# Optimization experiments

Hardware: AMD Instinct MI355X
Metric: run time of the kernel (lower is better)

The kernel has to match this reference:

```python
import jax, jax.numpy as jnp
import numpy as np

D_MODEL = 2048
NHEADS = 16
HEAD_DIM = D_MODEL // NHEADS


def setup_inputs() -> dict:
    key = jax.random.key(0)
    kx, kq, kk, kv, ko = jax.random.split(key, 5)
    B, S = 2, 2048
    scale = 1.0 / np.sqrt(D_MODEL)
    return {
        "x": jax.random.normal(kx, (B, S, D_MODEL), dtype=jnp.float32),
        "Wq": jax.random.normal(kq, (D_MODEL, D_MODEL), dtype=jnp.float32) * scale,
        "Wk": jax.random.normal(kk, (D_MODEL, D_MODEL), dtype=jnp.float32) * scale,
        "Wv": jax.random.normal(kv, (D_MODEL, D_MODEL), dtype=jnp.float32) * scale,
        "Wo": jax.random.normal(ko, (D_MODEL, D_MODEL), dtype=jnp.float32) * scale,
    }


def reference(x, Wq, Wk, Wv, Wo):
    B, S, _ = x.shape
    # nn.Linear(bias=False): y = x @ W.T
    q = (x @ Wq.T).reshape(B, S, NHEADS, HEAD_DIM)
    k = (x @ Wk.T).reshape(B, S, NHEADS, HEAD_DIM)
    v = (x @ Wv.T).reshape(B, S, NHEADS, HEAD_DIM)
    sm_scale = 1.0 / np.sqrt(HEAD_DIM)
    # scores: [B, H, S, S]
    scores = jnp.einsum("bqhd,bkhd->bhqk", q, k) * sm_scale
    causal_mask = jnp.tril(jnp.ones((S, S), dtype=bool))  # [S, S]
    scores = jnp.where(causal_mask, scores, jnp.finfo(scores.dtype).min)
    probs = jax.nn.softmax(scores, axis=-1)
    attn = jnp.einsum("bhqk,bkhd->bqhd", probs, v)  # [B, S, H, D]
    out = attn.reshape(B, S, D_MODEL) @ Wo.T
    return out
```

## Files before the change

kernel.cpp:

```cpp
#include <hip/hip_runtime.h>
#include <hip/hip_bf16.h>
#include <type_traits>

#define DEV __device__ __forceinline__

typedef __bf16 bf16x8 __attribute__((ext_vector_type(8)));
typedef float f32x4 __attribute__((ext_vector_type(4)));
typedef float f32x16 __attribute__((ext_vector_type(16)));
typedef unsigned short u16;
typedef unsigned int u32;

DEV u16 f32_to_bf16(float f) {
  union { float f; u32 u; } x; x.f = f;
  u32 r = (x.u + 0x7FFFu + ((x.u >> 16) & 1u)) >> 16;
  return (u16)r;
}

DEV u32 pack2(float a, float b) {
  union { __hip_bfloat162 h; u32 u; } c;
  c.h = __float22bfloat162_rn(float2{a, b});
  return c.u;
}

DEV void ld_lds16(const void* g, void* l) {
  __builtin_amdgcn_global_load_lds(
      (const __attribute__((address_space(1))) u32*)g,
      (__attribute__((address_space(3))) u32*)l, 16, 0, 0);
}

#define MFMA16(a, b, c) __builtin_amdgcn_mfma_f32_16x16x32_bf16(a, b, c, 0, 0, 0)
#define MFMA32(a, b, c) __builtin_amdgcn_mfma_f32_32x32x16_bf16(a, b, c, 0, 0, 0)

__global__ __launch_bounds__(256) void cast_kernel(const float* __restrict__ in,
                                                   u16* __restrict__ out, int n) {
  int i = (blockIdx.x * 256 + threadIdx.x) * 4;
  if (i >= n) return;
  float4 v = *reinterpret_cast<const float4*>(in + i);
  ushort4 o;
  o.x = f32_to_bf16(v.x); o.y = f32_to_bf16(v.y);
  o.z = f32_to_bf16(v.z); o.w = f32_to_bf16(v.w);
  *reinterpret_cast<ushort4*>(out + i) = o;
}

template <typename OutT>
__global__ __launch_bounds__(256) void gemm_nt(const u16* __restrict__ A,
                                               const u16* __restrict__ B,
                                               OutT* __restrict__ C,
                                               int M, int N, int K, float osc) {
  __shared__ __align__(16) u16 sA[128 * 64];
  __shared__ __align__(16) u16 sB[128 * 64];
  const int tid = threadIdx.x;
  const int lane = tid & 63, wid = tid >> 6;
  const int lo = lane & 15, hi = lane >> 4;
  const int wm = wid >> 1, wn = wid & 1;
  const int m0 = blockIdx.y * 128, n0 = blockIdx.x * 128;

  f32x4 acc[4][4] = {};

  for (int k0 = 0; k0 < K; k0 += 64) {
    __syncthreads();
#pragma unroll
    for (int i = 0; i < 4; ++i) {
      int e16 = i * 256 + tid;
      int r = e16 >> 3;
      int bcol = ((e16 & 7) * 16) ^ ((r & 7) << 4);
      int col = bcol >> 1;
      ld_lds16(A + (size_t)(m0 + r) * K + k0 + col, sA + e16 * 8);
      ld_lds16(B + (size_t)(n0 + r) * K + k0 + col, sB + e16 * 8);
    }
    __syncthreads();
#pragma unroll
    for (int kc = 0; kc < 2; ++kc) {
      bf16x8 a[4], b[4];
#pragma unroll
      for (int i = 0; i < 4; ++i) {
        int row = wm * 64 + i * 16 + lo;
        int boff = ((kc * 32 + hi * 8) * 2) ^ ((row & 7) << 4);
        a[i] = *(const bf16x8*)((const char*)sA + row * 128 + boff);
      }
#pragma unroll
      for (int i = 0; i < 4; ++i) {
        int row = wn * 64 + i * 16 + lo;
        int boff = ((kc * 32 + hi * 8) * 2) ^ ((row & 7) << 4);
        b[i] = *(const bf16x8*)((const char*)sB + row * 128 + boff);
      }
#pragma unroll
      for (int mi = 0; mi < 4; ++mi)
#pragma unroll
        for (int ni = 0; ni < 4; ++ni)
          acc[mi][ni] = MFMA16(a[mi], b[ni], acc[mi][ni]);
    }
  }
#pragma unroll
  for (int mi = 0; mi < 4; ++mi)
#pragma unroll
    for (int r = 0; r < 4; ++r) {
      size_t row = m0 + wm * 64 + mi * 16 + hi * 4 + r;
#pragma unroll
      for (int ni = 0; ni < 4; ++ni) {
        int col = n0 + wn * 64 + ni * 16 + lo;
        float v = acc[mi][ni][r] * osc;
        if constexpr (std::is_same<OutT, float>::value)
          C[row * N + col] = v;
        else
          C[row * N + col] = f32_to_bf16(v);
      }
    }
}

constexpr float RTHR2 = 11.5416f;

__global__ __launch_bounds__(512, 2) void attn_fwd(const u16* __restrict__ Q,
                                                   const u16* __restrict__ K,
                                                   const u16* __restrict__ VT,
                                                   u16* __restrict__ O) {
  __shared__ __align__(16) u16 sK[2][64 * 128];
  __shared__ __align__(16) u16 sV[2][128 * 64];

  const int p = blockIdx.x, h = blockIdx.y, b = blockIdx.z;
  const int tid = threadIdx.x;
  const int lane = tid & 63, wid = tid >> 6;
  const int l31 = lane & 31, hi5 = lane >> 5;
  const int g = wid >> 2;
  const int qt = g ? p : (15 - p);
  const int qw = qt * 128 + (wid & 3) * 32;
  const int qg = qw + l31;
  const int nt = 2 * (15 - p) + 2;

  const size_t baseQK = ((size_t)b * 2048) * 2048 + (size_t)h * 128;
  const size_t baseV  = ((size_t)h * 128) * 4096 + (size_t)b * 2048;

  bf16x8 qf[8];
#pragma unroll
  for (int kc = 0; kc < 8; ++kc)
    qf[kc] = *(const bf16x8*)(Q + baseQK + (size_t)qg * 2048 + kc * 16 + hi5 * 8);

  f32x16 o[4] = {};
  float m = -INFINITY, ls = 0.f;

  auto stage = [&](int buf, int t) {
    const int kv = t * 64;
#pragma unroll
    for (int i = 0; i < 2; ++i) {
      int e = i * 512 + tid;
      int r = e >> 4;
      int bc = ((e & 15) * 16) ^ ((r & 7) << 4);
      ld_lds16(K + baseQK + (size_t)(kv + r) * 2048 + (bc >> 1), &sK[buf][e * 8]);
    }
#pragma unroll
    for (int i = 0; i < 2; ++i) {
      int e = i * 512 + tid;
      int r = e >> 3;
      int bc = ((e & 7) * 16) ^ ((r & 7) << 4);
      ld_lds16(VT + baseV + (size_t)r * 4096 + kv + (bc >> 1), &sV[buf][e * 8]);
    }
  };

  stage(0, 0);

  for (int t = 0; t < nt; ++t) {
    __syncthreads();
    if (t + 1 < nt) stage((t + 1) & 1, t + 1);
    const int kv0 = t * 64;
    if (kv0 > qw + 31) continue;
    const u16* bK = sK[t & 1];
    const u16* bV = sV[t & 1];

    f32x16 s[2] = {};
    __builtin_amdgcn_s_setprio(1);
#pragma unroll
    for (int kb = 0; kb < 2; ++kb) {
      int row = kb * 32 + l31;
      int rsw = (row & 7) << 4;
#pragma unroll
      for (int kc = 0; kc < 8; ++kc) {
        int bo = (kc * 32 + hi5 * 16) ^ rsw;
        bf16x8 kf = *(const bf16x8*)((const char*)bK + row * 256 + bo);
        s[kb] = MFMA32(kf, qf[kc], s[kb]);
      }
    }
    __builtin_amdgcn_s_setprio(0);

    if (kv0 + 63 > qw) {
#pragma unroll
      for (int kb = 0; kb < 2; ++kb)
#pragma unroll
        for (int j = 0; j < 16; ++j) {
          int keyg = kv0 + kb * 32 + (j & 3) + 8 * (j >> 2) + 4 * hi5;
          s[kb][j] = (keyg > qg) ? -3e38f : s[kb][j];
        }
    }

    float pmax = -3e38f;
#pragma unroll
    for (int kb = 0; kb < 2; ++kb)
#pragma unroll
      for (int j = 0; j < 16; ++j) pmax = fmaxf(pmax, s[kb][j]);
    pmax = fmaxf(pmax, __shfl_xor(pmax, 32));

    if (!__all(pmax - m <= RTHR2)) {
      float mn = fmaxf(m, pmax);
      float fr = exp2f(m - mn);
      ls *= fr;
#pragma unroll
      for (int d = 0; d < 4; ++d) o[d] *= fr;
      m = mn;
    }

    float rs = 0.f;
#pragma unroll
    for (int kb = 0; kb < 2; ++kb)
#pragma unroll
      for (int j = 0; j < 16; ++j) {
        float pv = exp2f(s[kb][j] - m);
        s[kb][j] = pv;
        rs += pv;
      }
    rs += __shfl_xor(rs, 32);
    ls += rs;

    union PF { u32 w[4]; bf16x8 v; };
    PF pf[4];
#pragma unroll
    for (int kb = 0; kb < 2; ++kb)
#pragma unroll
      for (int gp = 0; gp < 2; ++gp) {
        u32 keep[2], send[2];
#pragma unroll
        for (int w = 0; w < 2; ++w) {
          int ja = 8 * gp + 2 * w;
          int jb = 8 * gp + 4 + 2 * w;
          u32 aa = pack2(s[kb][ja], s[kb][ja + 1]);
          u32 bb = pack2(s[kb][jb], s[kb][jb + 1]);
          keep[w] = hi5 ? bb : aa;
          send[w] = hi5 ? aa : bb;
        }
        u32 recv0 = (u32)__shfl_xor((int)send[0], 32);
        u32 recv1 = (u32)__shfl_xor((int)send[1], 32);
        PF& f = pf[2 * kb + gp];
        f.w[0] = hi5 ? recv0 : keep[0];
        f.w[1] = hi5 ? recv1 : keep[1];
        f.w[2] = hi5 ? keep[0] : recv0;
        f.w[3] = hi5 ? keep[1] : recv1;
      }

    __builtin_amdgcn_s_setprio(1);
#pragma unroll
    for (int d = 0; d < 4; ++d) {
      int row = d * 32 + l31;
      int rsw = (row & 7) << 4;
#pragma unroll
      for (int ks = 0; ks < 4; ++ks) {
        int bo = (ks * 32 + hi5 * 16) ^ rsw;
        bf16x8 vf = *(const bf16x8*)((const char*)bV + row * 128 + bo);
        o[d] = MFMA32(vf, pf[ks].v, o[d]);
      }
    }
    __builtin_amdgcn_s_setprio(0);
  }

  float inv = 1.f / ls;
  size_t orow = (size_t)b * 2048 + qg;
#pragma unroll
  for (int d = 0; d < 4; ++d)
#pragma unroll
    for (int G = 0; G < 4; ++G) {
      union { u32 u[2]; ushort4 s4; } st;
      st.u[0] = pack2(o[d][4 * G + 0] * inv, o[d][4 * G + 1] * inv);
      st.u[1] = pack2(o[d][4 * G + 2] * inv, o[d][4 * G + 3] * inv);
      int col = h * 128 + d * 32 + 8 * G + 4 * hi5;
      *(ushort4*)(O + orow * 2048 + col) = st.s4;
    }
}

extern "C" void kernel_launch(void* const* d_in, const int* in_sizes, int n_in,
                              void* d_out, int out_size, void* d_ws, size_t ws_size,
                              hipStream_t stream) {
  const float* x  = (const float*)d_in[0];
  const float* Wq = (const float*)d_in[1];
  const float* Wk = (const float*)d_in[2];
  const float* Wv = (const float*)d_in[3];
  const float* Wo = (const float*)d_in[4];
  float* out = (float*)d_out;

  constexpr int B = 2, S = 2048, D = 2048;
  constexpr int M = B * S;
  constexpr float QSC = 0.12751742f;

  char* ws = (char*)d_ws;
  u16* xb  = (u16*)ws; ws += (size_t)M * D * 2;
  u16* wqb = (u16*)ws; ws += (size_t)D * D * 2;
  u16* wkb = (u16*)ws; ws += (size_t)D * D * 2;
  u16* wvb = (u16*)ws; ws += (size_t)D * D * 2;
  u16* wob = (u16*)ws; ws += (size_t)D * D * 2;
  u16* q   = (u16*)ws; ws += (size_t)M * D * 2;
  u16* k   = (u16*)ws; ws += (size_t)M * D * 2;
  u16* vT  = (u16*)ws; ws += (size_t)M * D * 2;
  u16* att = (u16*)ws; ws += (size_t)M * D * 2;

  cast_kernel<<<M * D / 1024, 256, 0, stream>>>(x, xb, M * D);
  cast_kernel<<<D * D / 1024, 256, 0, stream>>>(Wq, wqb, D * D);
  cast_kernel<<<D * D / 1024, 256, 0, stream>>>(Wk, wkb, D * D);
  cast_kernel<<<D * D / 1024, 256, 0, stream>>>(Wv, wvb, D * D);
  cast_kernel<<<D * D / 1024, 256, 0, stream>>>(Wo, wob, D * D);

  dim3 gg(D / 128, M / 128);
  gemm_nt<u16><<<gg, 256, 0, stream>>>(xb, wqb, q, M, D, D, QSC);
  gemm_nt<u16><<<gg, 256, 0, stream>>>(xb, wkb, k, M, D, D, 1.0f);
  gemm_nt<u16><<<dim3(M / 128, D / 128), 256, 0, stream>>>(wvb, xb, vT, D, M, D, 1.0f);

  attn_fwd<<<dim3(8, 16, B), 512, 0, stream>>>(q, k, vT, att);

  gemm_nt<float><<<gg, 256, 0, stream>>>(att, wob, out, M, D, D, 1.0f);
}
```

Measured before the change: 286.8 us.

## Rewrite GEMM as 8-wave triple-buffered pipeline and split attention into single-tile blocks

New measurement: 315.8 us. 1.1x slower.

```diff
diff --git a/kernel.cpp b/kernel.cpp
--- a/kernel.cpp
+++ b/kernel.cpp
@@ -30,6 +30,12 @@
 
 #define MFMA16(a, b, c) __builtin_amdgcn_mfma_f32_16x16x32_bf16(a, b, c, 0, 0, 0)
 #define MFMA32(a, b, c) __builtin_amdgcn_mfma_f32_32x32x16_bf16(a, b, c, 0, 0, 0)
+#define BAR() __builtin_amdgcn_s_barrier()
+
+DEV bf16x8 rd_frag(const u16* s, int row, int kc, int hi) {
+  int bo = ((kc * 32 + hi * 8) * 2) ^ ((row & 7) << 4);
+  return *(const bf16x8*)((const char*)s + row * 128 + bo);
+}
 
 __global__ __launch_bounds__(256) void cast_kernel(const float* __restrict__ in,
                                                    u16* __restrict__ out, int n) {
@@ -43,54 +49,86 @@
 }
 
 template <typename OutT>
-__global__ __launch_bounds__(256) void gemm_nt(const u16* __restrict__ A,
-                                               const u16* __restrict__ B,
-                                               OutT* __restrict__ C,
-                                               int M, int N, int K, float osc) {
-  __shared__ __align__(16) u16 sA[128 * 64];
-  __shared__ __align__(16) u16 sB[128 * 64];
+__global__ __launch_bounds__(512) void gemm_nt8(const u16* __restrict__ A,
+                                                const u16* __restrict__ B,
+                                                OutT* __restrict__ C,
+                                                int M, int N, int K, float osc) {
+  __shared__ __align__(16) u16 sA[3][128 * 64];
+  __shared__ __align__(16) u16 sB[3][256 * 64];
   const int tid = threadIdx.x;
   const int lane = tid & 63, wid = tid >> 6;
   const int lo = lane & 15, hi = lane >> 4;
-  const int wm = wid >> 1, wn = wid & 1;
-  const int m0 = blockIdx.y * 128, n0 = blockIdx.x * 128;
+  const int wm = wid >> 2, wn = wid & 3;
+  const int m0 = blockIdx.y * 128, n0 = blockIdx.x * 256;
+  const int NT = K >> 6;
 
   f32x4 acc[4][4] = {};
 
-  for (int k0 = 0; k0 < K; k0 += 64) {
-    __syncthreads();
-#pragma unroll
-    for (int i = 0; i < 4; ++i) {
-      int e16 = i * 256 + tid;
-      int r = e16 >> 3;
-      int bcol = ((e16 & 7) * 16) ^ ((r & 7) << 4);
-      int col = bcol >> 1;
-      ld_lds16(A + (size_t)(m0 + r) * K + k0 + col, sA + e16 * 8);
-      ld_lds16(B + (size_t)(n0 + r) * K + k0 + col, sB + e16 * 8);
-    }
-    __syncthreads();
+  auto stageA = [&](int buf, int kcol, int i) {
+    int e = i * 512 + tid;
+    int r = e >> 3;
+    int bc = ((e & 7) * 16) ^ ((r & 7) << 4);
+    ld_lds16(A + (size_t)(m0 + r) * K + kcol + (bc >> 1), &sA[buf][e * 8]);
+  };
+  auto stageB = [&](int buf, int kcol, int i) {
+    int e = i * 512 + tid;
+    int r = e >> 3;
+    int bc = ((e & 7) * 16) ^ ((r & 7) << 4);
+    ld_lds16(B + (size_t)(n0 + r) * K + kcol + (bc >> 1), &sB[buf][e * 8]);
+  };
+
+  stageA(0, 0, 0);  stageA(0, 0, 1);
+  stageB(0, 0, 0);  stageB(0, 0, 1);  stageB(0, 0, 2);  stageB(0, 0, 3);
+  stageA(1, 64, 0); stageA(1, 64, 1);
+  stageB(1, 64, 0); stageB(1, 64, 1); stageB(1, 64, 2); stageB(1, 64, 3);
+
+  for (int t = 0; t < NT; ++t) {
+    const u16* cA = sA[t % 3];
+    const u16* cB = sB[t % 3];
+    const int nb = (t + 2) % 3;
+    const bool st = (t + 2) < NT;
+    const int tk = (t + 2) * 64;
+
+    if (t + 1 < NT) asm volatile("s_waitcnt vmcnt(6)" ::: "memory");
+    else            asm volatile("s_waitcnt vmcnt(0)" ::: "memory");
+    BAR();
+
 #pragma unroll
     for (int kc = 0; kc < 2; ++kc) {
-      bf16x8 a[4], b[4];
-#pragma unroll
-      for (int i = 0; i < 4; ++i) {
-        int row = wm * 64 + i * 16 + lo;
-        int boff = ((kc * 32 + hi * 8) * 2) ^ ((row & 7) << 4);
-        a[i] = *(const bf16x8*)((const char*)sA + row * 128 + boff);
-      }
-#pragma unroll
-      for (int i = 0; i < 4; ++i) {
-        int row = wn * 64 + i * 16 + lo;
-        int boff = ((kc * 32 + hi * 8) * 2) ^ ((row & 7) << 4);
-        b[i] = *(const bf16x8*)((const char*)sB + row * 128 + boff);
-      }
-#pragma unroll
-      for (int mi = 0; mi < 4; ++mi)
+      bf16x8 a01[2], bv[4], a23[2];
+#pragma unroll
+      for (int mi = 0; mi < 2; ++mi) a01[mi] = rd_frag(cA, wm * 64 + mi * 16 + lo, kc, hi);
+#pragma unroll
+      for (int ni = 0; ni < 4; ++ni) bv[ni] = rd_frag(cB, wn * 64 + ni * 16 + lo, kc, hi);
+      if (st) {
+        if (kc == 0) { stageA(nb, tk, 0); stageA(nb, tk, 1); }
+        else         { stageB(nb, tk, 2); stageB(nb, tk, 3); }
+      }
+      BAR();
+      __builtin_amdgcn_s_setprio(1);
+#pragma unroll
+      for (int mi = 0; mi < 2; ++mi)
 #pragma unroll
         for (int ni = 0; ni < 4; ++ni)
-          acc[mi][ni] = MFMA16(a[mi], b[ni], acc[mi][ni]);
+          acc[mi][ni] = MFMA16(a01[mi], bv[ni], acc[mi][ni]);
+      __builtin_amdgcn_s_setprio(0);
+      BAR();
+
+#pragma unroll
+      for (int mi = 0; mi < 2; ++mi) a23[mi] = rd_frag(cA, wm * 64 + (mi + 2) * 16 + lo, kc, hi);
+      if (st && kc == 0) { stageB(nb, tk, 0); stageB(nb, tk, 1); }
+      BAR();
+      __builtin_amdgcn_s_setprio(1);
+#pragma unroll
+      for (int mi = 0; mi < 2; ++mi)
+#pragma unroll
+        for (int ni = 0; ni < 4; ++ni)
+          acc[mi + 2][ni] = MFMA16(a23[mi], bv[ni], acc[mi + 2][ni]);
+      __builtin_amdgcn_s_setprio(0);
+      BAR();
     }
   }
+
 #pragma unroll
   for (int mi = 0; mi < 4; ++mi)
 #pragma unroll
@@ -110,25 +148,25 @@
 
 constexpr float RTHR2 = 11.5416f;
 
-__global__ __launch_bounds__(512, 2) void attn_fwd(const u16* __restrict__ Q,
+__global__ __launch_bounds__(256, 2) void attn_fwd(const u16* __restrict__ Q,
                                                    const u16* __restrict__ K,
                                                    const u16* __restrict__ VT,
                                                    u16* __restrict__ O) {
   __shared__ __align__(16) u16 sK[2][64 * 128];
   __shared__ __align__(16) u16 sV[2][128 * 64];
 
-  const int p = blockIdx.x, h = blockIdx.y, b = blockIdx.z;
+  const int x = blockIdx.x, h = blockIdx.y, b = blockIdx.z;
+  const int qt = b ? x : (15 - x);
   const int tid = threadIdx.x;
   const int lane = tid & 63, wid = tid >> 6;
   const int l31 = lane & 31, hi5 = lane >> 5;
-  const int g = wid >> 2;
-  const int qt = g ? p : (15 - p);
-  const int qw = qt * 128 + (wid & 3) * 32;
-  const int qg = qw + l31;
-  const int nt = 2 * (15 - p) + 2;
 
   const size_t baseQK = ((size_t)b * 2048) * 2048 + (size_t)h * 128;
   const size_t baseV  = ((size_t)h * 128) * 4096 + (size_t)b * 2048;
+  const int q0 = qt * 128;
+  const int qw = q0 + wid * 32;
+  const int qg = qw + l31;
+  const int nt = 2 * qt + 2;
 
   bf16x8 qf[8];
 #pragma unroll
@@ -141,15 +179,15 @@
   auto stage = [&](int buf, int t) {
     const int kv = t * 64;
 #pragma unroll
-    for (int i = 0; i < 2; ++i) {
-      int e = i * 512 + tid;
+    for (int i = 0; i < 4; ++i) {
+      int e = i * 256 + tid;
       int r = e >> 4;
       int bc = ((e & 15) * 16) ^ ((r & 7) << 4);
       ld_lds16(K + baseQK + (size_t)(kv + r) * 2048 + (bc >> 1), &sK[buf][e * 8]);
     }
 #pragma unroll
-    for (int i = 0; i < 2; ++i) {
-      int e = i * 512 + tid;
+    for (int i = 0; i < 4; ++i) {
+      int e = i * 256 + tid;
       int r = e >> 3;
       int bc = ((e & 7) * 16) ^ ((r & 7) << 4);
       ld_lds16(VT + baseV + (size_t)r * 4096 + kv + (bc >> 1), &sV[buf][e * 8]);
@@ -167,7 +205,6 @@
     const u16* bV = sV[t & 1];
 
     f32x16 s[2] = {};
-    __builtin_amdgcn_s_setprio(1);
 #pragma unroll
     for (int kb = 0; kb < 2; ++kb) {
       int row = kb * 32 + l31;
@@ -179,7 +216,6 @@
         s[kb] = MFMA32(kf, qf[kc], s[kb]);
       }
     }
-    __builtin_amdgcn_s_setprio(0);
 
     if (kv0 + 63 > qw) {
 #pragma unroll
@@ -244,7 +280,6 @@
         f.w[3] = hi5 ? keep[1] : recv1;
       }
 
-    __builtin_amdgcn_s_setprio(1);
 #pragma unroll
     for (int d = 0; d < 4; ++d) {
       int row = d * 32 + l31;
@@ -256,7 +291,6 @@
         o[d] = MFMA32(vf, pf[ks].v, o[d]);
       }
     }
-    __builtin_amdgcn_s_setprio(0);
   }
 
   float inv = 1.f / ls;
@@ -304,12 +338,12 @@
   cast_kernel<<<D * D / 1024, 256, 0, stream>>>(Wv, wvb, D * D);
   cast_kernel<<<D * D / 1024, 256, 0, stream>>>(Wo, wob, D * D);
 
-  dim3 gg(D / 128, M / 128);
-  gemm_nt<u16><<<gg, 256, 0, stream>>>(xb, wqb, q, M, D, D, QSC);
-  gemm_nt<u16><<<gg, 256, 0, stream>>>(xb, wkb, k, M, D, D, 1.0f);
-  gemm_nt<u16><<<dim3(M / 128, D / 128), 256, 0, stream>>>(wvb, xb, vT, D, M, D, 1.0f);
-
-  attn_fwd<<<dim3(8, 16, B), 512, 0, stream>>>(q, k, vT, att);
-
-  gemm_nt<float><<<gg, 256, 0, stream>>>(att, wob, out, M, D, D, 1.0f);
-}
+  dim3 gg(D / 256, M / 128);
+  gemm_nt8<u16><<<gg, 512, 0, stream>>>(xb, wqb, q, M, D, D, QSC);
+  gemm_nt8<u16><<<gg, 512, 0, stream>>>(xb, wkb, k, M, D, D, 1.0f);
+  gemm_nt8<u16><<<dim3(M / 256, D / 128), 512, 0, stream>>>(wvb, xb, vT, D, M, D, 1.0f);
+
+  attn_fwd<<<dim3(16, 16, B), 256, 0, stream>>>(q, k, vT, att);
+
+  gemm_nt8<float><<<gg, 512, 0, stream>>>(att, wob, out, M, D, D, 1.0f);
+}
```

## Fuse casts and Q/K projections; restructure attention with direct V register loads

Applied to the files above, without the earlier changes.

Result: no change. 285.6 us (-0.4%).

```diff
diff --git a/kernel.cpp b/kernel.cpp
--- a/kernel.cpp
+++ b/kernel.cpp
@@ -31,22 +31,33 @@
 #define MFMA16(a, b, c) __builtin_amdgcn_mfma_f32_16x16x32_bf16(a, b, c, 0, 0, 0)
 #define MFMA32(a, b, c) __builtin_amdgcn_mfma_f32_32x32x16_bf16(a, b, c, 0, 0, 0)
 
-__global__ __launch_bounds__(256) void cast_kernel(const float* __restrict__ in,
-                                                   u16* __restrict__ out, int n) {
-  int i = (blockIdx.x * 256 + threadIdx.x) * 4;
-  if (i >= n) return;
-  float4 v = *reinterpret_cast<const float4*>(in + i);
+__global__ __launch_bounds__(256) void cast_all(
+    const float* __restrict__ x,  const float* __restrict__ wq,
+    const float* __restrict__ wk, const float* __restrict__ wv,
+    const float* __restrict__ wo,
+    u16* __restrict__ xb,  u16* __restrict__ wqb, u16* __restrict__ wkb,
+    u16* __restrict__ wvb, u16* __restrict__ wob) {
+  int bid = blockIdx.x;
+  const float* src; u16* dst; int base;
+  if (bid < 8192)       { src = x;  dst = xb;  base = bid; }
+  else if (bid < 12288) { src = wq; dst = wqb; base = bid - 8192; }
+  else if (bid < 16384) { src = wk; dst = wkb; base = bid - 12288; }
+  else if (bid < 20480) { src = wv; dst = wvb; base = bid - 16384; }
+  else                  { src = wo; dst = wob; base = bid - 20480; }
+  int i = (base * 256 + threadIdx.x) * 4;
+  float4 v = *reinterpret_cast<const float4*>(src + i);
   ushort4 o;
   o.x = f32_to_bf16(v.x); o.y = f32_to_bf16(v.y);
   o.z = f32_to_bf16(v.z); o.w = f32_to_bf16(v.w);
-  *reinterpret_cast<ushort4*>(out + i) = o;
+  *reinterpret_cast<ushort4*>(dst + i) = o;
 }
 
 template <typename OutT>
 __global__ __launch_bounds__(256) void gemm_nt(const u16* __restrict__ A,
                                                const u16* __restrict__ B,
                                                OutT* __restrict__ C,
-                                               int M, int N, int K, float osc) {
+                                               int M, int N, int K,
+                                               float oscLo, float oscHi, int nsplit) {
   __shared__ __align__(16) u16 sA[128 * 64];
   __shared__ __align__(16) u16 sB[128 * 64];
   const int tid = threadIdx.x;
@@ -54,6 +65,7 @@
   const int lo = lane & 15, hi = lane >> 4;
   const int wm = wid >> 1, wn = wid & 1;
   const int m0 = blockIdx.y * 128, n0 = blockIdx.x * 128;
+  const float osc = (n0 < nsplit) ? oscLo : oscHi;
 
   f32x4 acc[4][4] = {};
 
@@ -110,30 +122,29 @@
 
 constexpr float RTHR2 = 11.5416f;
 
-__global__ __launch_bounds__(512, 2) void attn_fwd(const u16* __restrict__ Q,
-                                                   const u16* __restrict__ K,
+__global__ __launch_bounds__(256, 2) void attn_fwd(const u16* __restrict__ QK,
                                                    const u16* __restrict__ VT,
                                                    u16* __restrict__ O) {
   __shared__ __align__(16) u16 sK[2][64 * 128];
-  __shared__ __align__(16) u16 sV[2][128 * 64];
-
-  const int p = blockIdx.x, h = blockIdx.y, b = blockIdx.z;
+
+  const int x = blockIdx.x, h = blockIdx.y, b = blockIdx.z;
+  const int qt = b ? x : (15 - x);
   const int tid = threadIdx.x;
   const int lane = tid & 63, wid = tid >> 6;
   const int l31 = lane & 31, hi5 = lane >> 5;
-  const int g = wid >> 2;
-  const int qt = g ? p : (15 - p);
-  const int qw = qt * 128 + (wid & 3) * 32;
+
+  const size_t baseQ = ((size_t)b * 2048) * 4096 + (size_t)h * 128;
+  const size_t baseK = baseQ + 2048;
+  const size_t baseV = ((size_t)h * 128) * 4096 + (size_t)b * 2048;
+  const int q0 = qt * 128;
+  const int qw = q0 + wid * 32;
   const int qg = qw + l31;
-  const int nt = 2 * (15 - p) + 2;
-
-  const size_t baseQK = ((size_t)b * 2048) * 2048 + (size_t)h * 128;
-  const size_t baseV  = ((size_t)h * 128) * 4096 + (size_t)b * 2048;
+  const int nt = 2 * qt + 2;
 
   bf16x8 qf[8];
 #pragma unroll
   for (int kc = 0; kc < 8; ++kc)
-    qf[kc] = *(const bf16x8*)(Q + baseQK + (size_t)qg * 2048 + kc * 16 + hi5 * 8);
+    qf[kc] = *(const bf16x8*)(QK + baseQ + (size_t)qg * 4096 + kc * 16 + hi5 * 8);
 
   f32x16 o[4] = {};
   float m = -INFINITY, ls = 0.f;
@@ -141,18 +152,11 @@
   auto stage = [&](int buf, int t) {
     const int kv = t * 64;
 #pragma unroll
-    for (int i = 0; i < 2; ++i) {
-      int e = i * 512 + tid;
+    for (int i = 0; i < 4; ++i) {
+      int e = i * 256 + tid;
       int r = e >> 4;
       int bc = ((e & 15) * 16) ^ ((r & 7) << 4);
-      ld_lds16(K + baseQK + (size_t)(kv + r) * 2048 + (bc >> 1), &sK[buf][e * 8]);
-    }
-#pragma unroll
-    for (int i = 0; i < 2; ++i) {
-      int e = i * 512 + tid;
-      int r = e >> 3;
-      int bc = ((e & 7) * 16) ^ ((r & 7) << 4);
-      ld_lds16(VT + baseV + (size_t)r * 4096 + kv + (bc >> 1), &sV[buf][e * 8]);
+      ld_lds16(QK + baseK + (size_t)(kv + r) * 4096 + (bc >> 1), &sK[buf][e * 8]);
     }
   };
 
@@ -164,10 +168,8 @@
     const int kv0 = t * 64;
     if (kv0 > qw + 31) continue;
     const u16* bK = sK[t & 1];
-    const u16* bV = sV[t & 1];
 
     f32x16 s[2] = {};
-    __builtin_amdgcn_s_setprio(1);
 #pragma unroll
     for (int kb = 0; kb < 2; ++kb) {
       int row = kb * 32 + l31;
@@ -179,7 +181,14 @@
         s[kb] = MFMA32(kf, qf[kc], s[kb]);
       }
     }
-    __builtin_amdgcn_s_setprio(0);
+
+    bf16x8 vfr[4][4];
+#pragma unroll
+    for (int d = 0; d < 4; ++d)
+#pragma unroll
+      for (int ks = 0; ks < 4; ++ks)
+        vfr[d][ks] = *(const bf16x8*)(VT + baseV + (size_t)(d * 32 + l31) * 4096 +
+                                      kv0 + ks * 16 + hi5 * 8);
 
     if (kv0 + 63 > qw) {
 #pragma unroll
@@ -244,19 +253,11 @@
         f.w[3] = hi5 ? keep[1] : recv1;
       }
 
-    __builtin_amdgcn_s_setprio(1);
-#pragma unroll
-    for (int d = 0; d < 4; ++d) {
-      int row = d * 32 + l31;
-      int rsw = (row & 7) << 4;
-#pragma unroll
-      for (int ks = 0; ks < 4; ++ks) {
-        int bo = (ks * 32 + hi5 * 16) ^ rsw;
-        bf16x8 vf = *(const bf16x8*)((const char*)bV + row * 128 + bo);
-        o[d] = MFMA32(vf, pf[ks].v, o[d]);
-      }
-    }
-    __builtin_amdgcn_s_setprio(0);
+#pragma unroll
+    for (int d = 0; d < 4; ++d)
+#pragma unroll
+      for (int ks = 0; ks < 4; ++ks)
+        o[d] = MFMA32(vfr[d][ks], pf[ks].v, o[d]);
   }
 
   float inv = 1.f / ls;
@@ -293,23 +294,19 @@
   u16* wkb = (u16*)ws; ws += (size_t)D * D * 2;
   u16* wvb = (u16*)ws; ws += (size_t)D * D * 2;
   u16* wob = (u16*)ws; ws += (size_t)D * D * 2;
-  u16* q   = (u16*)ws; ws += (size_t)M * D * 2;
-  u16* k   = (u16*)ws; ws += (size_t)M * D * 2;
+  u16* qk  = (u16*)ws; ws += (size_t)M * 2 * D * 2;
   u16* vT  = (u16*)ws; ws += (size_t)M * D * 2;
   u16* att = (u16*)ws; ws += (size_t)M * D * 2;
 
-  cast_kernel<<<M * D / 1024, 256, 0, stream>>>(x, xb, M * D);
-  cast_kernel<<<D * D / 1024, 256, 0, stream>>>(Wq, wqb, D * D);
-  cast_kernel<<<D * D / 1024, 256, 0, stream>>>(Wk, wkb, D * D);
-  cast_kernel<<<D * D / 1024, 256, 0, stream>>>(Wv, wvb, D * D);
-  cast_kernel<<<D * D / 1024, 256, 0, stream>>>(Wo, wob, D * D);
-
-  dim3 gg(D / 128, M / 128);
-  gemm_nt<u16><<<gg, 256, 0, stream>>>(xb, wqb, q, M, D, D, QSC);
-  gemm_nt<u16><<<gg, 256, 0, stream>>>(xb, wkb, k, M, D, D, 1.0f);
-  gemm_nt<u16><<<dim3(M / 128, D / 128), 256, 0, stream>>>(wvb, xb, vT, D, M, D, 1.0f);
-
-  attn_fwd<<<dim3(8, 16, B), 512, 0, stream>>>(q, k, vT, att);
-
-  gemm_nt<float><<<gg, 256, 0, stream>>>(att, wob, out, M, D, D, 1.0f);
-}
+  cast_all<<<24576, 256, 0, stream>>>(x, Wq, Wk, Wv, Wo, xb, wqb, wkb, wvb, wob);
+
+  gemm_nt<u16><<<dim3(32, 32), 256, 0, stream>>>(xb, wqb, qk, M, 2 * D, D,
+                                                 QSC, 1.0f, D);
+  gemm_nt<u16><<<dim3(M / 128, D / 128), 256, 0, stream>>>(wvb, xb, vT, D, M, D,
+                                                           1.0f, 1.0f, 1 << 30);
+
+  attn_fwd<<<dim3(16, 16, B), 256, 0, stream>>>(qk, vT, att);
+
+  gemm_nt<float><<<dim3(D / 128, M / 128), 256, 0, stream>>>(att, wob, out, M, D, D,
+                                                             1.0f, 1.0f, 1 << 30);
+}
```
